# Kernel optimization log

Hardware: AMD Instinct MI355X
Metric: run time of the kernel (lower is better)

Reference implementation:

```python
import jax, jax.numpy as jnp
import numpy as np
import math

B, N, C = 16, 4096, 256
WS = 8            # window_size
NH = 8            # num_heads
HD = C // NH      # head_dim = 32
LK = 32           # linformer compressed length
G = 16            # global bank tokens


def setup_inputs() -> dict:
    key = jax.random.key(0)
    ks = jax.random.split(key, 10)
    x = jax.random.normal(ks[0], (B, N, C), dtype=jnp.float32)
    W_qkv = jax.random.normal(ks[1], (C, 3 * C), dtype=jnp.float32) * 0.02
    b_qkv = jnp.zeros((3 * C,), dtype=jnp.float32)
    E_k = jax.random.normal(ks[2], (WS * WS, LK), dtype=jnp.float32) * 0.02
    E_v = jax.random.normal(ks[3], (WS * WS, LK), dtype=jnp.float32) * 0.02
    k_bank = jax.random.normal(ks[4], (G, C), dtype=jnp.float32)
    v_bank = jax.random.normal(ks[5], (G, C), dtype=jnp.float32)
    W_proj = jax.random.normal(ks[6], (C, C), dtype=jnp.float32) * 0.02
    b_proj = jnp.zeros((C,), dtype=jnp.float32)
    return {"x": x, "W_qkv": W_qkv, "b_qkv": b_qkv, "E_k": E_k, "E_v": E_v,
            "k_bank": k_bank, "v_bank": v_bank, "W_proj": W_proj, "b_proj": b_proj,
            "window_size": WS, "num_heads": NH}


def reference(x, W_qkv, b_qkv, E_k, E_v, k_bank, v_bank, W_proj, b_proj, window_size, num_heads):
    Bb, Nn, Cc = x.shape
    Hs = int(math.isqrt(Nn))          # H = W = sqrt(N), divisible by window_size here
    ws = window_size
    nh = Hs // ws                      # windows per side
    hd = Cc // num_heads
    NW = ws * ws                       # tokens per window

    # ---- window partition: [B,N,C] -> [BW, NW, C]
    xw = x.reshape(Bb, nh, ws, nh, ws, Cc).transpose(0, 1, 3, 2, 4, 5)
    xw = xw.reshape(Bb * nh * nh, NW, Cc)
    BW = xw.shape[0]

    # ---- qkv projection and head split: (3, BW, H, NW, hd)
    qkv = (xw @ W_qkv + b_qkv).reshape(BW, NW, 3, num_heads, hd)
    qkv = qkv.transpose(2, 0, 3, 1, 4)
    q, k, v = qkv[0], qkv[1], qkv[2]

    # ---- Linformer KV compression: NW == seq_len (no pad branch)
    k_c = jnp.einsum('nk,bhnd->bhkd', E_k, k)   # [BW,H,LK,hd]
    v_c = jnp.einsum('nk,bhnd->bhkd', E_v, v)

    # ---- global memory bank, broadcast to all windows: [BW,H,G,hd]
    Gt = k_bank.shape[0]
    kb = jnp.broadcast_to(k_bank.reshape(Gt, num_heads, hd).transpose(1, 0, 2)[None],
                          (BW, num_heads, Gt, hd))
    vb = jnp.broadcast_to(v_bank.reshape(Gt, num_heads, hd).transpose(1, 0, 2)[None],
                          (BW, num_heads, Gt, hd))

    k_full = jnp.concatenate([k_c, kb], axis=2)  # [BW,H,LK+G,hd]
    v_full = jnp.concatenate([v_c, vb], axis=2)

    # ---- SDPA (dropout_p = 0)
    scale = 1.0 / math.sqrt(hd)
    scores = jnp.einsum('bhqd,bhkd->bhqk', q, k_full) * scale
    attn = jax.nn.softmax(scores, axis=-1)
    out = jnp.einsum('bhqk,bhkd->bhqd', attn, v_full)     # [BW,H,NW,hd]

    out = out.transpose(0, 2, 1, 3).reshape(BW, NW, Cc)
    out = out @ W_proj + b_proj

    # ---- window reverse: [BW,NW,C] -> [B,N,C]
    out = out.reshape(Bb, nh, nh, ws, ws, Cc).transpose(0, 1, 3, 2, 4, 5)
    out = out.reshape(Bb, Hs * Hs, Cc)
    return out
```

## Files before the change

kernel.cpp:

```cpp
#include <hip/hip_runtime.h>
#include <hip/hip_bf16.h>


typedef unsigned int uint;
typedef __attribute__((ext_vector_type(8))) short short8;
typedef __attribute__((ext_vector_type(4))) float f32x4;
typedef __attribute__((ext_vector_type(4))) uint uintx4;

__device__ __forceinline__ float bup(uint hs) {
    return __uint_as_float(hs << 16);
}
__device__ __forceinline__ uint f2b(float f) {
    __hip_bfloat16 h = __float2bfloat16(f);
    unsigned short u;
    __builtin_memcpy(&u, &h, 2);
    return (uint)u;
}
__device__ __forceinline__ uint f2b2(float a, float b) {
    __hip_bfloat162 h = __float22bfloat162_rn(make_float2(a, b));
    uint u;
    __builtin_memcpy(&u, &h, 4);
    return u;
}
__device__ __forceinline__ f32x4 mfma16(short8 a, short8 b, f32x4 c) {
    return __builtin_amdgcn_mfma_f32_16x16x32_bf16(a, b, c, 0, 0, 0);
}
__device__ __forceinline__ int sw256(int r, int c) { return r * 256 + (c ^ ((r & 7) << 3)); }

__device__ __forceinline__ short8 xpose(f32x4 a, f32x4 b, float s, int lane) {
    const uint pa0 = f2b2(a[0] * s, a[1] * s), pa1 = f2b2(a[2] * s, a[3] * s);
    const uint pb0 = f2b2(b[0] * s, b[1] * s), pb1 = f2b2(b[2] * s, b[3] * s);
    const int s0 = ((lane >> 4) & 1) * 32 + (lane & 15);
    const int s1 = s0 + 16;
    const uint w0a = __shfl(pa0, s0), w0b = __shfl(pb0, s0);
    const uint w1a = __shfl(pa1, s0), w1b = __shfl(pb1, s0);
    const uint w2a = __shfl(pa0, s1), w2b = __shfl(pb0, s1);
    const uint w3a = __shfl(pa1, s1), w3b = __shfl(pb1, s1);
    const bool hi = lane >= 32;
    uintx4 u;
    u[0] = hi ? w0b : w0a;
    u[1] = hi ? w1b : w1a;
    u[2] = hi ? w2b : w2a;
    u[3] = hi ? w3b : w3a;
    short8 r;
    __builtin_memcpy(&r, &u, 16);
    return r;
}

#define WS_WHQ 0
#define WS_WHP 196608
#define WS_WLP 262144
#define WS_EKT 327680
#define WS_EVT 329728
#define WS_KBF 331776
#define WS_VBF 335872

__global__ void __launch_bounds__(256)
eswa_prep(const float* __restrict__ Wqkv, const float* __restrict__ Wproj,
          const float* __restrict__ Ek, const float* __restrict__ Ev,
          const float* __restrict__ kbank, const float* __restrict__ vbank,
          short* __restrict__ wsp)
{
    const int blk = blockIdx.x, thr = threadIdx.x;
    if (blk < 192) {
        const int jh = blk & 1;
        const int g = (blk >> 1) * 256 + thr;
        const int lane = g & 63, tk = (g >> 6) & 7, tn = g >> 9;
        const int quad = lane >> 4, l16 = lane & 15;
        const int c = tn * 16 + l16;
        const int r0 = tk * 32 + quad * 8 + jh * 4;
        const float w0 = Wqkv[(r0 + 0) * 768 + c], w1 = Wqkv[(r0 + 1) * 768 + c];
        const float w2 = Wqkv[(r0 + 2) * 768 + c], w3 = Wqkv[(r0 + 3) * 768 + c];
        *(uint2*)(wsp + WS_WHQ + ((tn * 8 + tk) * 64 + lane) * 8 + jh * 4) =
            make_uint2(f2b2(w0, w1), f2b2(w2, w3));
    } else if (blk < 256) {
        const int idx = blk - 192, jh = idx & 1;
        const int g = (idx >> 1) * 256 + thr;
        const int lane = g & 63, tk = (g >> 6) & 7, tn = g >> 9;
        const int quad = lane >> 4, l16 = lane & 15;
        const int c = tn * 16 + l16;
        const int r0 = tk * 32 + quad * 8 + jh * 4;
        float w[4];
        #pragma unroll
        for (int j = 0; j < 4; ++j) w[j] = Wproj[(r0 + j) * 256 + c];
        const uint h01 = f2b2(w[0], w[1]), h23 = f2b2(w[2], w[3]);
        const float l0 = w[0] - bup(h01 & 0xffffu), l1 = w[1] - bup(h01 >> 16);
        const float l2 = w[2] - bup(h23 & 0xffffu), l3 = w[3] - bup(h23 >> 16);
        const int o = ((tn * 8 + tk) * 64 + lane) * 8 + jh * 4;
        *(uint2*)(wsp + WS_WHP + o) = make_uint2(h01, h23);
        *(uint2*)(wsp + WS_WLP + o) = make_uint2(f2b2(l0, l1), f2b2(l2, l3));
    } else if (blk < 258) {
        const float* E = (blk == 256) ? Ek : Ev;
        const int base = (blk == 256) ? WS_EKT : WS_EVT;
        const int lane = thr & 63, tk = (thr >> 6) & 1, tm = (thr >> 7) & 1;
        const int quad = lane >> 4, l16 = lane & 15;
        const int lk = tm * 16 + l16;
        uint pk[4];
        #pragma unroll
        for (int jp = 0; jp < 4; ++jp) {
            const int t = tk * 32 + quad * 8 + jp * 2;
            pk[jp] = f2b2(E[t * 32 + lk], E[(t + 1) * 32 + lk]);
        }
        *(uint4*)(wsp + base + ((tm * 2 + tk) * 64 + lane) * 8) =
            make_uint4(pk[0], pk[1], pk[2], pk[3]);
    } else {
        for (int idx = thr; idx < 512; idx += 256) {
            const int hh = idx >> 6, l = idx & 63;
            const int l16 = l & 15, q = l >> 4;
            uint pk[4];
            #pragma unroll
            for (int jp = 0; jp < 4; ++jp)
                pk[jp] = f2b2(kbank[l16 * 256 + hh * 32 + q * 8 + jp * 2],
                              kbank[l16 * 256 + hh * 32 + q * 8 + jp * 2 + 1]);
            *(uint4*)(wsp + WS_KBF + idx * 8) = make_uint4(pk[0], pk[1], pk[2], pk[3]);
        }
        for (int idx = thr; idx < 1024; idx += 256) {
            const int hh = idx >> 7, md = (idx >> 6) & 1, l = idx & 63;
            const int l16 = l & 15, q = l >> 4;
            uint pk[4] = {0u, 0u, 0u, 0u};
            if (q < 2) {
                #pragma unroll
                for (int jp = 0; jp < 4; ++jp)
                    pk[jp] = f2b2(vbank[(q * 8 + jp * 2) * 256 + hh * 32 + md * 16 + l16],
                                  vbank[(q * 8 + jp * 2 + 1) * 256 + hh * 32 + md * 16 + l16]);
            }
            *(uint4*)(wsp + WS_VBF + idx * 8) = make_uint4(pk[0], pk[1], pk[2], pk[3]);
        }
    }
}

#define SMEM_BYTES 49152

__global__ void __launch_bounds__(512, 4)
eswa_main(const float* __restrict__ x, const float* __restrict__ bqkv,
          const float* __restrict__ bproj, const short* __restrict__ wsp,
          float* __restrict__ out)
{
    extern __shared__ char smem[];
    short* xh   = (short*)smem;
    short* attn = (short*)smem + 8192;

    const int tid  = threadIdx.x;
    const int wave = tid >> 6;
    const int lane = tid & 63;
    const int quad = lane >> 4;
    const int l16  = lane & 15;
    const int h    = wave;

    const int b  = blockIdx.x >> 6;
    const int w  = blockIdx.x & 63;
    const int rw = w >> 3;
    const int cw = w & 7;

    #pragma unroll
    for (int i = 0; i < 8; ++i) {
        const int vi = tid + 512 * i;
        const int t  = vi >> 6;
        const int c  = (vi & 63) * 4;
        const int n  = (rw * 8 + (t >> 3)) * 64 + cw * 8 + (t & 7);
        const float4 xv = *(const float4*)(x + (size_t)(b * 4096 + n) * 256 + c);
        *(uint2*)(xh + sw256(t, c)) = make_uint2(f2b2(xv.x, xv.y), f2b2(xv.z, xv.w));
    }
    __syncthreads();

    const short* WF = wsp + WS_WHQ;

    short8 kfr[2][2], vfr[2][2];
    {
        f32x4 acc[2][4];
        #pragma unroll
        for (int nd = 0; nd < 2; ++nd) {
            const float bk = bqkv[256 + h * 32 + nd * 16 + l16];
            #pragma unroll
            for (int mt = 0; mt < 4; ++mt) acc[nd][mt] = (f32x4){bk, bk, bk, bk};
        }
        #pragma unroll 2
        for (int tk = 0; tk < 8; ++tk) {
            short8 xf[4];
            #pragma unroll
            for (int mt = 0; mt < 4; ++mt)
                xf[mt] = *(const short8*)(xh + sw256(mt * 16 + l16, tk * 32 + quad * 8));
            #pragma unroll
            for (int nd = 0; nd < 2; ++nd) {
                const short8 wf =
                    *(const short8*)(WF + (((16 + h * 2 + nd) * 8 + tk) * 64 + lane) * 8);
                #pragma unroll
                for (int mt = 0; mt < 4; ++mt) acc[nd][mt] = mfma16(xf[mt], wf, acc[nd][mt]);
            }
        }
        #pragma unroll
        for (int nd = 0; nd < 2; ++nd)
            #pragma unroll
            for (int kk = 0; kk < 2; ++kk)
                kfr[nd][kk] = xpose(acc[nd][2 * kk], acc[nd][2 * kk + 1], 1.0f, lane);
    }
    {
        f32x4 acc[2][4];
        #pragma unroll
        for (int nd = 0; nd < 2; ++nd) {
            const float bv = bqkv[512 + h * 32 + nd * 16 + l16];
            #pragma unroll
            for (int mt = 0; mt < 4; ++mt) acc[nd][mt] = (f32x4){bv, bv, bv, bv};
        }
        #pragma unroll 2
        for (int tk = 0; tk < 8; ++tk) {
            short8 xf[4];
            #pragma unroll
            for (int mt = 0; mt < 4; ++mt)
                xf[mt] = *(const short8*)(xh + sw256(mt * 16 + l16, tk * 32 + quad * 8));
            #pragma unroll
            for (int nd = 0; nd < 2; ++nd) {
                const short8 wf =
                    *(const short8*)(WF + (((32 + h * 2 + nd) * 8 + tk) * 64 + lane) * 8);
                #pragma unroll
                for (int mt = 0; mt < 4; ++mt) acc[nd][mt] = mfma16(xf[mt], wf, acc[nd][mt]);
            }
        }
        #pragma unroll
        for (int nd = 0; nd < 2; ++nd)
            #pragma unroll
            for (int kk = 0; kk < 2; ++kk)
                vfr[nd][kk] = xpose(acc[nd][2 * kk], acc[nd][2 * kk + 1], 1.0f, lane);
    }
    short8 kcf[2], vcf[2];
    {
        short8 ekf[2][2], evf[2][2];
        #pragma unroll
        for (int tm = 0; tm < 2; ++tm)
            #pragma unroll
            for (int kk = 0; kk < 2; ++kk) {
                ekf[tm][kk] = *(const short8*)(wsp + WS_EKT + ((tm * 2 + kk) * 64 + lane) * 8);
                evf[tm][kk] = *(const short8*)(wsp + WS_EVT + ((tm * 2 + kk) * 64 + lane) * 8);
            }
        f32x4 ck[2][2];
        #pragma unroll
        for (int md = 0; md < 2; ++md)
            #pragma unroll
            for (int nl = 0; nl < 2; ++nl) ck[md][nl] = (f32x4){0, 0, 0, 0};
        #pragma unroll
        for (int kk = 0; kk < 2; ++kk)
            #pragma unroll
            for (int md = 0; md < 2; ++md)
                #pragma unroll
                for (int nl = 0; nl < 2; ++nl)
                    ck[md][nl] = mfma16(kfr[md][kk], ekf[nl][kk], ck[md][nl]);
        #pragma unroll
        for (int nl = 0; nl < 2; ++nl)
            kcf[nl] = xpose(ck[0][nl], ck[1][nl], 1.0f, lane);
        f32x4 cv[2][2];
        #pragma unroll
        for (int ml = 0; ml < 2; ++ml)
            #pragma unroll
            for (int nd = 0; nd < 2; ++nd) cv[ml][nd] = (f32x4){0, 0, 0, 0};
        #pragma unroll
        for (int kk = 0; kk < 2; ++kk)
            #pragma unroll
            for (int ml = 0; ml < 2; ++ml)
                #pragma unroll
                for (int nd = 0; nd < 2; ++nd)
                    cv[ml][nd] = mfma16(evf[ml][kk], vfr[nd][kk], cv[ml][nd]);
        #pragma unroll
        for (int nd = 0; nd < 2; ++nd)
            vcf[nd] = xpose(cv[0][nd], cv[1][nd], 1.0f, lane);
    }
    const short8 kbf = *(const short8*)(wsp + WS_KBF + (h * 64 + lane) * 8);
    short8 vbf[2];
    #pragma unroll
    for (int md = 0; md < 2; ++md)
        vbf[md] = *(const short8*)(wsp + WS_VBF + ((h * 2 + md) * 64 + lane) * 8);

    short8 qfr[4];
    {
        f32x4 acc[2][4];
        #pragma unroll
        for (int md = 0; md < 2; ++md) {
            const float4 bq = *(const float4*)(bqkv + h * 32 + md * 16 + quad * 4);
            #pragma unroll
            for (int nt = 0; nt < 4; ++nt) acc[md][nt] = (f32x4){bq.x, bq.y, bq.z, bq.w};
        }
        #pragma unroll 2
        for (int tk = 0; tk < 8; ++tk) {
            short8 xf[4];
            #pragma unroll
            for (int nt = 0; nt < 4; ++nt)
                xf[nt] = *(const short8*)(xh + sw256(nt * 16 + l16, tk * 32 + quad * 8));
            #pragma unroll
            for (int md = 0; md < 2; ++md) {
                const short8 wf =
                    *(const short8*)(WF + (((h * 2 + md) * 8 + tk) * 64 + lane) * 8);
                #pragma unroll
                for (int nt = 0; nt < 4; ++nt) acc[md][nt] = mfma16(wf, xf[nt], acc[md][nt]);
            }
        }
        #pragma unroll
        for (int nt = 0; nt < 4; ++nt)
            qfr[nt] = xpose(acc[0][nt], acc[1][nt], 0.17677669529663687f, lane);
    }
    __syncthreads();

    short* scr = (short*)smem + wave * 1024;
    if (lane >= 32) {
        const int ch = (64 + lane) ^ ((lane >> 3) & 7);
        *(uint4*)(scr + ch * 8) = make_uint4(0, 0, 0, 0);
    }
    const int rdx0 = (lane ^ ((lane >> 3) & 7)) * 8;
    const int rdx1 = ((64 + lane) ^ ((lane >> 3) & 7)) * 8;

    #pragma unroll
    for (int th = 0; th < 2; ++th) {
        f32x4 sc[2][3];
        #pragma unroll
        for (int mt = 0; mt < 2; ++mt) {
            const short8 qa = qfr[th * 2 + mt];
            sc[mt][0] = mfma16(qa, kcf[0], (f32x4){0, 0, 0, 0});
            sc[mt][1] = mfma16(qa, kcf[1], (f32x4){0, 0, 0, 0});
            sc[mt][2] = mfma16(qa, kbf,    (f32x4){0, 0, 0, 0});
        }
        float inv[2][4];
        #pragma unroll
        for (int mt = 0; mt < 2; ++mt) {
            #pragma unroll
            for (int r = 0; r < 4; ++r) {
                float mm = fmaxf(fmaxf(sc[mt][0][r], sc[mt][1][r]), sc[mt][2][r]);
                mm = fmaxf(mm, __shfl_xor(mm, 1));
                mm = fmaxf(mm, __shfl_xor(mm, 2));
                mm = fmaxf(mm, __shfl_xor(mm, 4));
                mm = fmaxf(mm, __shfl_xor(mm, 8));
                const float e0 = __expf(sc[mt][0][r] - mm);
                const float e1 = __expf(sc[mt][1][r] - mm);
                const float e2 = __expf(sc[mt][2][r] - mm);
                sc[mt][0][r] = e0; sc[mt][1][r] = e1; sc[mt][2][r] = e2;
                float su = e0 + e1 + e2;
                su += __shfl_xor(su, 1);
                su += __shfl_xor(su, 2);
                su += __shfl_xor(su, 4);
                su += __shfl_xor(su, 8);
                inv[mt][r] = 1.0f / su;
            }
        }
        #pragma unroll
        for (int mt = 0; mt < 2; ++mt) {
            #pragma unroll
            for (int nk = 0; nk < 3; ++nk) {
                const int qt = (nk * 2 + (l16 >> 3)) & 3;
                const int kk = nk >> 1;
                const int xr = (qt * 2 + (quad >> 1)) & 7;
                #pragma unroll
                for (int r = 0; r < 4; ++r) {
                    const int ch = (kk * 64 + qt * 16 + quad * 4 + r) ^ xr;
                    scr[ch * 8 + (l16 & 7)] = (short)f2b(sc[mt][nk][r] * inv[mt][r]);
                }
            }
            asm volatile("s_waitcnt lgkmcnt(0)" ::: "memory");
            __builtin_amdgcn_sched_barrier(0);
            const short8 pa0 = *(const short8*)(scr + rdx0);
            const short8 pa1 = *(const short8*)(scr + rdx1);
            #pragma unroll
            for (int md = 0; md < 2; ++md) {
                f32x4 o = mfma16(vcf[md], pa0, (f32x4){0, 0, 0, 0});
                o = mfma16(vbf[md], pa1, o);
                *(uint2*)(attn + sw256((th * 2 + mt) * 16 + l16,
                                       h * 32 + md * 16 + quad * 4)) =
                    make_uint2(f2b2(o[0], o[1]), f2b2(o[2], o[3]));
            }
        }
    }
    __syncthreads();

    {
        const short* Whp = wsp + WS_WHP;
        const short* Wlp = wsp + WS_WLP;
        f32x4 acc[2][4];
        #pragma unroll
        for (int p = 0; p < 2; ++p) {
            const float bi = bproj[(wave * 2 + p) * 16 + l16];
            #pragma unroll
            for (int m = 0; m < 4; ++m) acc[p][m] = (f32x4){bi, bi, bi, bi};
        }
        #pragma unroll 2
        for (int tk = 0; tk < 8; ++tk) {
            short8 aA[4];
            #pragma unroll
            for (int m = 0; m < 4; ++m)
                aA[m] = *(const short8*)(attn + sw256(m * 16 + l16, tk * 32 + quad * 8));
            #pragma unroll
            for (int p = 0; p < 2; ++p) {
                const int bo = (((wave * 2 + p) * 8 + tk) * 64 + lane) * 8;
                const short8 bh = *(const short8*)(Whp + bo);
                const short8 bl = *(const short8*)(Wlp + bo);
                #pragma unroll
                for (int m = 0; m < 4; ++m) {
                    acc[p][m] = mfma16(aA[m], bh, acc[p][m]);
                    acc[p][m] = mfma16(aA[m], bl, acc[p][m]);
                }
            }
        }
        #pragma unroll
        for (int p = 0; p < 2; ++p)
            #pragma unroll
            for (int m = 0; m < 4; ++m)
                #pragma unroll
                for (int r = 0; r < 4; ++r) {
                    const int t = m * 16 + quad * 4 + r;
                    const int n = (rw * 8 + (t >> 3)) * 64 + cw * 8 + (t & 7);
                    out[(size_t)(b * 4096 + n) * 256 + (wave * 2 + p) * 16 + l16] =
                        acc[p][m][r];
                }
    }
}

extern "C" void kernel_launch(void* const* d_in, const int* in_sizes, int n_in,
                              void* d_out, int out_size, void* d_ws, size_t ws_size,
                              hipStream_t stream) {
    const float* x     = (const float*)d_in[0];
    const float* Wqkv  = (const float*)d_in[1];
    const float* bqkv  = (const float*)d_in[2];
    const float* Ek    = (const float*)d_in[3];
    const float* Ev    = (const float*)d_in[4];
    const float* kbank = (const float*)d_in[5];
    const float* vbank = (const float*)d_in[6];
    const float* Wproj = (const float*)d_in[7];
    const float* bproj = (const float*)d_in[8];
    float* outp        = (float*)d_out;
    short* wsp         = (short*)d_ws;
    (void)in_sizes; (void)n_in; (void)out_size; (void)ws_size;

    (void)hipFuncSetAttribute((const void*)eswa_main,
                              hipFuncAttributeMaxDynamicSharedMemorySize, SMEM_BYTES);

    eswa_prep<<<259, 256, 0, stream>>>(Wqkv, Wproj, Ek, Ev, kbank, vbank, wsp);
    eswa_main<<<1024, 512, SMEM_BYTES, stream>>>(x, bqkv, bproj, wsp, outp);
}
```

Measured before the change: 186.3 us.

## Compute transposed scores and use register xpose instead of LDS scratch for P

Swaps the MFMA operands so scores come out with keys along rows, letting the softmax reductions use two cross-quad shuffles instead of four. The probability matrix is then repacked into B-operand layout with the existing in-register xpose helper rather than being written to and read back from a per-wave LDS scratch buffer. This also lets the attention output alias the x buffer, dropping shared memory from 48KB to 32KB. It relies on xpose producing the correct fragment layout for the PV MFMA, and the aliasing depends on xh no longer being read after the preceding barrier.

```diff
diff --git a/kernel.cpp b/kernel.cpp
--- a/kernel.cpp
+++ b/kernel.cpp
@@ -129,7 +129,7 @@
     }
 }
 
-#define SMEM_BYTES 49152
+#define SMEM_BYTES 32768
 
 __global__ void __launch_bounds__(512, 4)
 eswa_main(const float* __restrict__ x, const float* __restrict__ bqkv,
@@ -138,7 +138,7 @@
 {
     extern __shared__ char smem[];
     short* xh   = (short*)smem;
-    short* attn = (short*)smem + 8192;
+    short* attn = (short*)smem;
 
     const int tid  = threadIdx.x;
     const int wave = tid >> 6;
@@ -298,71 +298,40 @@
     }
     __syncthreads();
 
-    short* scr = (short*)smem + wave * 1024;
-    if (lane >= 32) {
-        const int ch = (64 + lane) ^ ((lane >> 3) & 7);
-        *(uint4*)(scr + ch * 8) = make_uint4(0, 0, 0, 0);
-    }
-    const int rdx0 = (lane ^ ((lane >> 3) & 7)) * 8;
-    const int rdx1 = ((64 + lane) ^ ((lane >> 3) & 7)) * 8;
-
+    const f32x4 zero4 = (f32x4){0, 0, 0, 0};
     #pragma unroll
-    for (int th = 0; th < 2; ++th) {
-        f32x4 sc[2][3];
-        #pragma unroll
-        for (int mt = 0; mt < 2; ++mt) {
-            const short8 qa = qfr[th * 2 + mt];
-            sc[mt][0] = mfma16(qa, kcf[0], (f32x4){0, 0, 0, 0});
-            sc[mt][1] = mfma16(qa, kcf[1], (f32x4){0, 0, 0, 0});
-            sc[mt][2] = mfma16(qa, kbf,    (f32x4){0, 0, 0, 0});
-        }
-        float inv[2][4];
-        #pragma unroll
-        for (int mt = 0; mt < 2; ++mt) {
+    for (int tt = 0; tt < 4; ++tt) {
+        f32x4 sc[3];
+        sc[0] = mfma16(kcf[0], qfr[tt], zero4);
+        sc[1] = mfma16(kcf[1], qfr[tt], zero4);
+        sc[2] = mfma16(kbf,    qfr[tt], zero4);
+        float mm = sc[0][0];
+        #pragma unroll
+        for (int n = 0; n < 3; ++n)
+            #pragma unroll
+            for (int r = 0; r < 4; ++r) mm = fmaxf(mm, sc[n][r]);
+        mm = fmaxf(mm, __shfl_xor(mm, 16));
+        mm = fmaxf(mm, __shfl_xor(mm, 32));
+        float su = 0.0f;
+        #pragma unroll
+        for (int n = 0; n < 3; ++n)
             #pragma unroll
             for (int r = 0; r < 4; ++r) {
-                float mm = fmaxf(fmaxf(sc[mt][0][r], sc[mt][1][r]), sc[mt][2][r]);
-                mm = fmaxf(mm, __shfl_xor(mm, 1));
-                mm = fmaxf(mm, __shfl_xor(mm, 2));
-                mm = fmaxf(mm, __shfl_xor(mm, 4));
-                mm = fmaxf(mm, __shfl_xor(mm, 8));
-                const float e0 = __expf(sc[mt][0][r] - mm);
-                const float e1 = __expf(sc[mt][1][r] - mm);
-                const float e2 = __expf(sc[mt][2][r] - mm);
-                sc[mt][0][r] = e0; sc[mt][1][r] = e1; sc[mt][2][r] = e2;
-                float su = e0 + e1 + e2;
-                su += __shfl_xor(su, 1);
-                su += __shfl_xor(su, 2);
-                su += __shfl_xor(su, 4);
-                su += __shfl_xor(su, 8);
-                inv[mt][r] = 1.0f / su;
-            }
-        }
-        #pragma unroll
-        for (int mt = 0; mt < 2; ++mt) {
-            #pragma unroll
-            for (int nk = 0; nk < 3; ++nk) {
-                const int qt = (nk * 2 + (l16 >> 3)) & 3;
-                const int kk = nk >> 1;
-                const int xr = (qt * 2 + (quad >> 1)) & 7;
-                #pragma unroll
-                for (int r = 0; r < 4; ++r) {
-                    const int ch = (kk * 64 + qt * 16 + quad * 4 + r) ^ xr;
-                    scr[ch * 8 + (l16 & 7)] = (short)f2b(sc[mt][nk][r] * inv[mt][r]);
-                }
-            }
-            asm volatile("s_waitcnt lgkmcnt(0)" ::: "memory");
-            __builtin_amdgcn_sched_barrier(0);
-            const short8 pa0 = *(const short8*)(scr + rdx0);
-            const short8 pa1 = *(const short8*)(scr + rdx1);
-            #pragma unroll
-            for (int md = 0; md < 2; ++md) {
-                f32x4 o = mfma16(vcf[md], pa0, (f32x4){0, 0, 0, 0});
-                o = mfma16(vbf[md], pa1, o);
-                *(uint2*)(attn + sw256((th * 2 + mt) * 16 + l16,
-                                       h * 32 + md * 16 + quad * 4)) =
-                    make_uint2(f2b2(o[0], o[1]), f2b2(o[2], o[3]));
-            }
+                const float e = __expf(sc[n][r] - mm);
+                sc[n][r] = e;
+                su += e;
+            }
+        su += __shfl_xor(su, 16);
+        su += __shfl_xor(su, 32);
+        const float inv = 1.0f / su;
+        const short8 pa0 = xpose(sc[0], sc[1], inv, lane);
+        const short8 pa1 = xpose(sc[2], zero4, inv, lane);
+        #pragma unroll
+        for (int md = 0; md < 2; ++md) {
+            f32x4 o = mfma16(vcf[md], pa0, zero4);
+            o = mfma16(vbf[md], pa1, o);
+            *(uint2*)(attn + sw256(tt * 16 + l16, h * 32 + md * 16 + quad * 4)) =
+                make_uint2(f2b2(o[0], o[1]), f2b2(o[2], o[3]));
         }
     }
     __syncthreads();
```

New measurement: 176.6 us. 1.05x faster.
